# Kernel tuning notes

Measured on AMD Instinct MI355X. Metric: run time of the kernel, lower is better.

Reference implementation:

```python
import jax, jax.numpy as jnp
import numpy as np

# MolFormer TestBert config (from checkpoint hyper_parameters)
B, T, D, H, L, F, V = 64, 250, 768, 12, 12, 32, 2362
DH = D // H  # head dim = 64
EPS = 1e-6   # fast_transformers LinearAttention eps


def _layernorm(x, g, b):
    m = x.mean(-1, keepdims=True)
    v = ((x - m) ** 2).mean(-1, keepdims=True)
    return (x - m) / jnp.sqrt(v + 1e-5) * g + b


def setup_inputs() -> dict:
    key = jax.random.key(0)
    ks = jax.random.split(key, 20)
    s = 0.02

    def n(k, shape, scale=s):
        return jax.random.normal(k, shape, dtype=jnp.float32) * scale

    mask = jax.random.randint(ks[1], (B, T), 0, 2).astype(bool)
    mask = mask.at[:, 0].set(True)  # keep CLS position valid
    return {
        "batch": jax.random.randint(ks[0], (B, T), 0, V),
        "mask": mask,
        "tok_emb": n(ks[2], (V, D)),
        "pos_emb": n(ks[3], (1, T, D)),
        "Wq": n(ks[4], (L, D, D)), "bq": jnp.zeros((L, D)),
        "Wk": n(ks[5], (L, D, D)), "bk": jnp.zeros((L, D)),
        "Wv": n(ks[6], (L, D, D)), "bv": jnp.zeros((L, D)),
        "Wo": n(ks[7], (L, D, D)), "bo": jnp.zeros((L, D)),
        # GeneralizedRandomFeatures random projection omega: [L, head_dim, n_feats]
        "omega": jax.random.normal(ks[8], (L, DH, F), dtype=jnp.float32),
        "ln1_g": jnp.ones((L, D)), "ln1_b": jnp.zeros((L, D)),
        "ln2_g": jnp.ones((L, D)), "ln2_b": jnp.zeros((L, D)),
        # feed_forward_dimensions == n_embd in the builder kwargs
        "W1": n(ks[9], (L, D, D)), "b1": jnp.zeros((L, D)),
        "W2": n(ks[10], (L, D, D)), "b2": jnp.zeros((L, D)),
    }


def reference(batch, mask, tok_emb, pos_emb, Wq, bq, Wk, bk, Wv, bv, Wo, bo,
              omega, ln1_g, ln1_b, ln2_g, ln2_b, W1, b1, W2, b2):
    Bc, Tc = batch.shape
    # LengthMask(mask.sum(-1)) -> prefix key mask
    lengths = mask.astype(jnp.int32).sum(-1)
    key_mask = (jnp.arange(Tc)[None, :] < lengths[:, None]).astype(jnp.float32)  # [B,T]

    x = tok_emb[batch] + pos_emb[:, :Tc, :]  # dropout = identity in eval
    attn_w = None
    for l in range(L):
        q = (x @ Wq[l] + bq[l]).reshape(Bc, Tc, H, DH)
        k = (x @ Wk[l] + bk[l]).reshape(Bc, Tc, H, DH)
        v = (x @ Wv[l] + bv[l]).reshape(Bc, Tc, H, DH)
        # GeneralizedRandomFeatures: phi(x) = relu(x @ omega)
        Qf = jax.nn.relu(jnp.einsum('bthd,df->bthf', q, omega[l]))
        Kf = jax.nn.relu(jnp.einsum('bshd,df->bshf', k, omega[l]))
        Kf = Kf * key_mask[:, :, None, None]
        # linear attention: out = phi(Q) (phi(K)^T V) / (phi(Q) . sum phi(K))
        KV = jnp.einsum('bshf,bshm->bhfm', Kf, v)
        Z = 1.0 / (jnp.einsum('bthf,bhf->bth', Qf, Kf.sum(axis=1)) + EPS)
        out = jnp.einsum('bthf,bhfm,bth->bthm', Qf, KV, Z)
        if l == L - 1:
            # 'linearwweights': the implied (normalized) attention matrix
            attn_w = jnp.einsum('bthf,bshf,bth->bhts', Qf, Kf, Z)
        out = out.reshape(Bc, Tc, D) @ Wo[l] + bo[l]
        # fast_transformers post-norm encoder layer
        x = _layernorm(x + out, ln1_g[l], ln1_b[l])
        y = jax.nn.gelu(x @ W1[l] + b1[l], approximate=False) @ W2[l] + b2[l]
        x = _layernorm(x + y, ln2_g[l], ln2_b[l])
    # mode == 'cls'
    return x[:, 0, :], attn_w
```

## Files before the change

### kernel.cpp

```cpp
#include <hip/hip_runtime.h>
#include <hip/hip_bf16.h>

typedef __hip_bfloat16 bf16;
typedef __attribute__((ext_vector_type(4))) float f32x4;
typedef __attribute__((ext_vector_type(8))) short bf16x8;
typedef __attribute__((ext_vector_type(4))) short short4v;

#define B_ 64
#define T_ 250
#define D_ 768
#define H_ 12
#define DH_ 64
#define F_ 32
#define L_ 12
#define BT_ (B_*T_)
#define BT_P 16128
#define NF_ (H_*F_)
#define QKVN_ (3*D_)
#define KVTN_ 80

static __device__ __forceinline__ float b2f(short s) {
    union { float f; unsigned u; } z; z.u = ((unsigned)(unsigned short)s) << 16; return z.f;
}
static __device__ __forceinline__ short f2bs(float f) {
    bf16 b = __float2bfloat16(f);
    return *(short*)&b;
}

__global__ void lengths_kernel(const unsigned char* __restrict__ mask, int* __restrict__ lengths) {
    __shared__ int not_i32, not_f32;
    const unsigned int* w = (const unsigned int*)mask;
    int tid = threadIdx.x;
    if (tid == 0) { not_i32 = 0; not_f32 = 0; }
    __syncthreads();
    int li = 0, lf = 0;
    for (int i = tid; i < 4000; i += 256) {
        unsigned int v = w[i];
        if (v > 1u) li = 1;
        if (v != 0u && v != 0x3F800000u) lf = 1;
    }
    if (li) not_i32 = 1;
    if (lf) not_f32 = 1;
    __syncthreads();
    int mode = (!not_i32) ? 0 : ((!not_f32) ? 1 : 2);
    if (tid < B_) {
        int cnt = 0;
        if (mode == 0) {
            const int* r = (const int*)mask + tid * T_;
            for (int t = 0; t < T_; ++t) cnt += (r[t] != 0);
        } else if (mode == 1) {
            const unsigned int* r = w + tid * T_;
            for (int t = 0; t < T_; ++t) cnt += (r[t] != 0);
        } else {
            const unsigned char* r = mask + tid * T_;
            for (int t = 0; t < T_; ++t) cnt += (r[t] != 0);
        }
        lengths[tid] = cnt;
    }
}

__global__ void embed_kernel(const int* __restrict__ batch, const float* __restrict__ tok,
                             const float* __restrict__ pos, float* __restrict__ x,
                             bf16* __restrict__ xb) {
    int bt = blockIdx.x;
    int t = bt % T_;
    int tok_id = batch[bt];
    const float* tr = tok + (size_t)tok_id * D_;
    const float* pr = pos + (size_t)t * D_;
    float* xr = x + (size_t)bt * D_;
    bf16* xbr = xb + (size_t)bt * D_;
    for (int d = threadIdx.x; d < D_; d += 256) {
        float v = tr[d] + pr[d];
        xr[d] = v;
        xbr[d] = __float2bfloat16(v);
    }
}

__global__ __launch_bounds__(256) void transpose_w_all(
    const float* __restrict__ Wq, const float* __restrict__ Wk, const float* __restrict__ Wv,
    const float* __restrict__ Wo, const float* __restrict__ W1, const float* __restrict__ W2,
    bf16* __restrict__ Wt)
{
    __shared__ float tile[32][33];
    int zz = blockIdx.z;
    int l = zz / 6, m = zz - l * 6;
    const float* src;
    switch (m) {
        case 0: src = Wq; break; case 1: src = Wk; break; case 2: src = Wv; break;
        case 3: src = Wo; break; case 4: src = W1; break; default: src = W2; break;
    }
    src += (size_t)l * D_ * D_;
    bf16* dst = Wt + (size_t)zz * D_ * D_;
    int k0 = blockIdx.y * 32, n0 = blockIdx.x * 32;
    int tx = threadIdx.x, ty = threadIdx.y;
#pragma unroll
    for (int i = 0; i < 4; ++i)
        tile[ty + i * 8][tx] = src[(size_t)(k0 + ty + i * 8) * D_ + n0 + tx];
    __syncthreads();
#pragma unroll
    for (int i = 0; i < 4; ++i)
        dst[(size_t)(n0 + ty + i * 8) * D_ + k0 + tx] = __float2bfloat16(tile[tx][ty + i * 8]);
}

__global__ void pack_bias(const float* __restrict__ bq, const float* __restrict__ bk,
                          const float* __restrict__ bv, float* __restrict__ qkvb) {
    int o = blockIdx.x * 256 + threadIdx.x;
    if (o >= L_ * QKVN_) return;
    int l = o / QKVN_, c = o - l * QKVN_;
    float v;
    if (c < D_) v = bq[l * D_ + c];
    else if (c < 2 * D_) v = bk[l * D_ + c - D_];
    else v = bv[l * D_ + c - 2 * D_];
    qkvb[o] = v;
}

#define GP_SLOT 28672
__global__ __launch_bounds__(512, 2) void gemm_pipe(
    const bf16* __restrict__ A, const bf16* __restrict__ Bt,
    const float* __restrict__ bias, bf16* __restrict__ C,
    int N, int lda, int ldc, int act, const int* __restrict__ lengths)
{
    __shared__ __attribute__((aligned(16))) short lds_s[2 * GP_SLOT];
    const int tid = threadIdx.x, lane = tid & 63, wave = tid >> 6;
    const int wm = wave >> 2, wn = wave & 3;
    const int rsel = lane & 15, kq = lane >> 4;

    const int gx = gridDim.x;
    const int nwg = gx * gridDim.y;
    int orig = blockIdx.y * gx + blockIdx.x;
    int q = nwg >> 3, r = nwg & 7;
    int xcd = orig & 7, idx = orig >> 3;
    int swz = (xcd < r) ? xcd * (q + 1) + idx : r * (q + 1) + (xcd - r) * q + idx;
    const int row0 = (swz / gx) * 256;
    const int col0 = (swz % gx) * 192;

    const int srow = wave * 8 + (lane >> 3);
    const int sblk = (lane & 7) ^ ((lane >> 3) & 7);
    const short* gA = (const short*)A + (size_t)(row0 + srow) * lda + sblk * 8;
    const short* gB = (const short*)Bt + (size_t)(col0 + srow) * 768 + sblk * 8;
    const int ldest = wave * 512;

    f32x4 acc[8][3];
#pragma unroll
    for (int i = 0; i < 8; ++i)
#pragma unroll
        for (int j = 0; j < 3; ++j) acc[i][j] = (f32x4){0.f, 0.f, 0.f, 0.f};

    auto STAGE = [&](int kt, int slot) {
        short* base = lds_s + slot * GP_SLOT;
        int kc = kt * 64;
#pragma unroll
        for (int j = 0; j < 4; ++j)
            __builtin_amdgcn_global_load_lds(
                (const __attribute__((address_space(1))) unsigned int*)(gA + (size_t)(j * 64) * lda + kc),
                (__attribute__((address_space(3))) unsigned int*)(base + j * 4096 + ldest), 16, 0, 0);
#pragma unroll
        for (int j = 0; j < 3; ++j)
            __builtin_amdgcn_global_load_lds(
                (const __attribute__((address_space(1))) unsigned int*)(gB + (size_t)(j * 64) * 768 + kc),
                (__attribute__((address_space(3))) unsigned int*)(base + 16384 + j * 4096 + ldest), 16, 0, 0);
    };

    auto COMPUTE = [&](int slot) {
        const short* sA = lds_s + slot * GP_SLOT;
        const short* sB = sA + 16384;
#pragma unroll
        for (int ks = 0; ks < 2; ++ks) {
            int kb = ks * 4 + kq;
            bf16x8 bv[3];
#pragma unroll
            for (int n = 0; n < 3; ++n) {
                int rowb = wn * 48 + n * 16 + rsel;
                bv[n] = *(const bf16x8*)(sB + rowb * 64 + ((kb ^ (rowb & 7)) << 3));
            }
#pragma unroll
            for (int mh = 0; mh < 2; ++mh) {
                bf16x8 av[4];
#pragma unroll
                for (int m2 = 0; m2 < 4; ++m2) {
                    int rowa = wm * 128 + (mh * 4 + m2) * 16 + rsel;
                    av[m2] = *(const bf16x8*)(sA + rowa * 64 + ((kb ^ (rowa & 7)) << 3));
                }
                __builtin_amdgcn_s_setprio(1);
#pragma unroll
                for (int m2 = 0; m2 < 4; ++m2)
#pragma unroll
                    for (int n = 0; n < 3; ++n)
                        acc[mh * 4 + m2][n] = __builtin_amdgcn_mfma_f32_16x16x32_bf16(
                            av[m2], bv[n], acc[mh * 4 + m2][n], 0, 0, 0);
                __builtin_amdgcn_s_setprio(0);
            }
        }
    };

    STAGE(0, 0); STAGE(1, 1);
    asm volatile("s_waitcnt vmcnt(7)" ::: "memory");
    __builtin_amdgcn_s_barrier();

    for (int t = 0; t < 12; ++t) {
        COMPUTE(t & 1);
        if (t < 11) {
            __builtin_amdgcn_s_barrier();
            if (t < 10) {
                STAGE(t + 2, t & 1);
                asm volatile("s_waitcnt vmcnt(7)" ::: "memory");
            } else {
                asm volatile("s_waitcnt vmcnt(0)" ::: "memory");
            }
            __builtin_amdgcn_s_barrier();
        }
    }

    float bj[3];
#pragma unroll
    for (int n = 0; n < 3; ++n) {
        int col = col0 + wn * 48 + n * 16 + rsel;
        bj[n] = bias ? bias[col] : 0.f;
    }
#pragma unroll
    for (int mi = 0; mi < 8; ++mi) {
#pragma unroll
        for (int rr = 0; rr < 4; ++rr) {
            int row = row0 + wm * 128 + mi * 16 + (kq << 2) + rr;
            bool kill = false;
            if (act == 3) { int b = row / T_; int t = row - b * T_; kill = (t >= lengths[b & 63]); }
            size_t base = (size_t)row * ldc + col0 + wn * 48 + rsel;
#pragma unroll
            for (int n = 0; n < 3; ++n) {
                float v = acc[mi][n][rr] + bj[n];
                if (act == 1) v = 0.5f * v * (1.0f + erff(v * 0.70710678118654752f));
                else if (act >= 2) v = fmaxf(v, 0.f);
                if (kill) v = 0.f;
                C[base + n * 16] = __float2bfloat16(v);
            }
        }
    }
}

__global__ __launch_bounds__(256) void feat_kernel(
    const bf16* __restrict__ qkv, const float* __restrict__ om,
    bf16* __restrict__ Qf, bf16* __restrict__ Kf, const int* __restrict__ lengths)
{
    __shared__ __attribute__((aligned(16))) short omT[32 * 64];
    int z = blockIdx.z, h = blockIdx.y;
    int row0 = blockIdx.x * 128;
    int tid = threadIdx.x, lane = tid & 63, wave = tid >> 6;
    {
        int f = tid >> 3, k0 = (tid & 7) * 8;
#pragma unroll
        for (int j = 0; j < 8; ++j)
            omT[f * 64 + k0 + j] = f2bs(om[(size_t)(k0 + j) * F_ + f]);
    }
    __syncthreads();

    const short* A = (const short*)qkv + (size_t)z * D_ + h * DH_;
    int rsel = lane & 15, kof = (lane >> 4) << 3;

    bf16x8 af[2][2], bfr[2][2];
#pragma unroll
    for (int mi = 0; mi < 2; ++mi) {
        int row = row0 + wave * 32 + mi * 16 + rsel;
#pragma unroll
        for (int ks = 0; ks < 2; ++ks)
            af[mi][ks] = *(const bf16x8*)(A + (size_t)row * QKVN_ + ks * 32 + kof);
    }
#pragma unroll
    for (int ni = 0; ni < 2; ++ni)
#pragma unroll
        for (int ks = 0; ks < 2; ++ks)
            bfr[ni][ks] = *(const bf16x8*)(omT + (ni * 16 + rsel) * 64 + ks * 32 + kof);

    f32x4 acc[2][2];
#pragma unroll
    for (int i = 0; i < 2; ++i)
#pragma unroll
        for (int j = 0; j < 2; ++j) acc[i][j] = (f32x4){0.f, 0.f, 0.f, 0.f};
#pragma unroll
    for (int mi = 0; mi < 2; ++mi)
#pragma unroll
        for (int ni = 0; ni < 2; ++ni)
#pragma unroll
            for (int ks = 0; ks < 2; ++ks)
                acc[mi][ni] = __builtin_amdgcn_mfma_f32_16x16x32_bf16(af[mi][ks], bfr[ni][ks], acc[mi][ni], 0, 0, 0);

    bf16* out = z ? Kf : Qf;
#pragma unroll
    for (int mi = 0; mi < 2; ++mi) {
#pragma unroll
        for (int r = 0; r < 4; ++r) {
            int row = row0 + wave * 32 + mi * 16 + ((lane >> 4) << 2) + r;
            bool kill = false;
            if (z) { int b = row / T_; int t = row - b * T_; kill = (t >= lengths[b]); }
#pragma unroll
            for (int ni = 0; ni < 2; ++ni) {
                float v = fmaxf(acc[mi][ni][r], 0.f);
                if (kill) v = 0.f;
                out[(size_t)row * NF_ + h * F_ + ni * 16 + rsel] = __float2bfloat16(v);
            }
        }
    }
}

__global__ __launch_bounds__(256) void kvsum_kernel(
    const bf16* __restrict__ Kf, const bf16* __restrict__ v, int ldv,
    bf16* __restrict__ KVt)
{
    __shared__ short KfS[64][36];
    __shared__ short vS[64][68];
    int h = blockIdx.x, b = blockIdx.y;
    int tid = threadIdx.x, lane = tid & 63, wv = tid >> 6;
    int lr = tid >> 2, cp = tid & 3;

    const short* Kg = (const short*)Kf + (size_t)(b * T_) * NF_ + h * F_;
    const short* Vg = (const short*)v + (size_t)(b * T_) * ldv + h * DH_;

    f32x4 acc[2];
    acc[0] = (f32x4){0.f, 0.f, 0.f, 0.f};
    acc[1] = (f32x4){0.f, 0.f, 0.f, 0.f};
    float ksacc = 0.f;

    for (int s0 = 0; s0 < T_; s0 += 64) {
        __syncthreads();
        int s = s0 + lr;
        if (s < T_) {
            bf16x8 k8 = *(const bf16x8*)(Kg + (size_t)s * NF_ + cp * 8);
            *(short4v*)&KfS[lr][cp * 8]     = *((const short4v*)&k8);
            *(short4v*)&KfS[lr][cp * 8 + 4] = *((const short4v*)&k8 + 1);
            bf16x8 v8a = *(const bf16x8*)(Vg + (size_t)s * ldv + cp * 16);
            bf16x8 v8b = *(const bf16x8*)(Vg + (size_t)s * ldv + cp * 16 + 8);
            *(short4v*)&vS[lr][cp * 16]      = *((const short4v*)&v8a);
            *(short4v*)&vS[lr][cp * 16 + 4]  = *((const short4v*)&v8a + 1);
            *(short4v*)&vS[lr][cp * 16 + 8]  = *((const short4v*)&v8b);
            *(short4v*)&vS[lr][cp * 16 + 12] = *((const short4v*)&v8b + 1);
        } else {
            short4v zz = (short4v){0, 0, 0, 0};
            *(short4v*)&KfS[lr][cp * 8]     = zz;
            *(short4v*)&KfS[lr][cp * 8 + 4] = zz;
            *(short4v*)&vS[lr][cp * 16]      = zz;
            *(short4v*)&vS[lr][cp * 16 + 4]  = zz;
            *(short4v*)&vS[lr][cp * 16 + 8]  = zz;
            *(short4v*)&vS[lr][cp * 16 + 12] = zz;
        }
        __syncthreads();
        if (tid < 32) {
            float p0 = 0.f, p1 = 0.f;
            for (int ss = 0; ss < 64; ss += 2) {
                p0 += b2f(KfS[ss][tid]);
                p1 += b2f(KfS[ss + 1][tid]);
            }
            ksacc += p0 + p1;
        }
        bf16x8 af0[2], af1[2], bfr[2];
#pragma unroll
        for (int ks = 0; ks < 2; ++ks) {
            int sb = ks * 32 + ((lane >> 4) << 3);
#pragma unroll
            for (int j = 0; j < 8; ++j) {
                ((short*)&af0[ks])[j] = KfS[sb + j][lane & 15];
                ((short*)&af1[ks])[j] = KfS[sb + j][16 + (lane & 15)];
                ((short*)&bfr[ks])[j] = vS[sb + j][wv * 16 + (lane & 15)];
            }
        }
#pragma unroll
        for (int ks = 0; ks < 2; ++ks) {
            acc[0] = __builtin_amdgcn_mfma_f32_16x16x32_bf16(af0[ks], bfr[ks], acc[0], 0, 0, 0);
            acc[1] = __builtin_amdgcn_mfma_f32_16x16x32_bf16(af1[ks], bfr[ks], acc[1], 0, 0, 0);
        }
    }

    bf16* dst = KVt + (size_t)(b * H_ + h) * KVTN_ * F_;
    int m = wv * 16 + (lane & 15);
#pragma unroll
    for (int mi = 0; mi < 2; ++mi) {
#pragma unroll
        for (int r = 0; r < 4; ++r) {
            int f = mi * 16 + ((lane >> 4) << 2) + r;
            dst[(size_t)m * F_ + f] = __float2bfloat16(acc[mi][r]);
        }
    }
    if (tid < 32) dst[(size_t)64 * F_ + tid] = __float2bfloat16(ksacc);
    if (tid < 240) {
        ((short*)dst)[65 * F_ + tid * 2]     = 0;
        ((short*)dst)[65 * F_ + tid * 2 + 1] = 0;
    }
}

__global__ __launch_bounds__(256) void attn_mfma(
    const bf16* __restrict__ Qf, const bf16* __restrict__ KVt,
    float* __restrict__ Z, bf16* __restrict__ out, int ldo)
{
    int h = blockIdx.x, b = blockIdx.y;
    int tid = threadIdx.x, lane = tid & 63, wv = tid >> 6;
    int t0 = wv * 64;
    int rsel = lane & 15, kof = (lane >> 4) << 3;

    const short* Qg = (const short*)Qf + h * F_;
    const short* Bg = (const short*)KVt + (size_t)(b * H_ + h) * KVTN_ * F_;

    bf16x8 af[4], bfr[5];
#pragma unroll
    for (int mi = 0; mi < 4; ++mi) {
        int t = t0 + mi * 16 + rsel;
        if (t > T_ - 1) t = T_ - 1;
        af[mi] = *(const bf16x8*)(Qg + (size_t)(b * T_ + t) * NF_ + kof);
    }
#pragma unroll
    for (int ni = 0; ni < 5; ++ni)
        bfr[ni] = *(const bf16x8*)(Bg + (size_t)(ni * 16 + rsel) * F_ + kof);

    f32x4 acc[4][5];
#pragma unroll
    for (int i = 0; i < 4; ++i)
#pragma unroll
        for (int j = 0; j < 5; ++j) acc[i][j] = (f32x4){0.f, 0.f, 0.f, 0.f};
#pragma unroll
    for (int mi = 0; mi < 4; ++mi)
#pragma unroll
        for (int ni = 0; ni < 5; ++ni)
            acc[mi][ni] = __builtin_amdgcn_mfma_f32_16x16x32_bf16(af[mi], bfr[ni], acc[mi][ni], 0, 0, 0);

#pragma unroll
    for (int mi = 0; mi < 4; ++mi) {
#pragma unroll
        for (int r = 0; r < 4; ++r) {
            int t = t0 + mi * 16 + ((lane >> 4) << 2) + r;
            float zden = __shfl(acc[mi][4][r], lane & 48, 64);
            float z = 1.0f / (zden + 1e-6f);
            if (t < T_) {
                if (rsel == 0) Z[(size_t)(b * T_ + t) * H_ + h] = z;
                size_t base = (size_t)(b * T_ + t) * ldo + h * DH_ + rsel;
#pragma unroll
                for (int ni = 0; ni < 4; ++ni)
                    out[base + ni * 16] = __float2bfloat16(acc[mi][ni][r] * z);
            }
        }
    }
}

__global__ __launch_bounds__(256) void attnw_kernel(const bf16* __restrict__ Qf,
                                                    const bf16* __restrict__ Kf,
                                                    const float* __restrict__ Z,
                                                    float* __restrict__ out) {
    int tt = blockIdx.x;
    int bh = blockIdx.y;
    int b = bh / H_, h = bh - b * H_;
    int tid = threadIdx.x;
    int lane = tid & 63, w = tid >> 6;
    int t0 = tt * 64, s0 = w * 64;
    int kof = (lane >> 4) * 8;

    const short* Qs = (const short*)Qf;
    const short* Ks = (const short*)Kf;

    bf16x8 af[4], bfr[4];
#pragma unroll
    for (int mi = 0; mi < 4; ++mi) {
        int t = t0 + mi * 16 + (lane & 15);
        if (t > T_ - 1) t = T_ - 1;
        af[mi] = *(const bf16x8*)(Qs + ((size_t)(b * T_ + t) * H_ + h) * F_ + kof);
    }
#pragma unroll
    for (int ni = 0; ni < 4; ++ni) {
        int s = s0 + ni * 16 + (lane & 15);
        if (s > T_ - 1) s = T_ - 1;
        bfr[ni] = *(const bf16x8*)(Ks + ((size_t)(b * T_ + s) * H_ + h) * F_ + kof);
    }

    f32x4 acc[4][4];
#pragma unroll
    for (int i = 0; i < 4; ++i)
#pragma unroll
        for (int j = 0; j < 4; ++j) acc[i][j] = (f32x4){0.f, 0.f, 0.f, 0.f};
#pragma unroll
    for (int mi = 0; mi < 4; ++mi)
#pragma unroll
        for (int ni = 0; ni < 4; ++ni)
            acc[mi][ni] = __builtin_amdgcn_mfma_f32_16x16x32_bf16(af[mi], bfr[ni], acc[mi][ni], 0, 0, 0);

#pragma unroll
    for (int mi = 0; mi < 4; ++mi) {
#pragma unroll
        for (int r = 0; r < 4; ++r) {
            int t = t0 + mi * 16 + (lane >> 4) * 4 + r;
            if (t >= T_) continue;
            float z = Z[(size_t)(b * T_ + t) * H_ + h];
            size_t base = ((size_t)bh * T_ + t) * T_;
#pragma unroll
            for (int ni = 0; ni < 4; ++ni) {
                int s = s0 + ni * 16 + (lane & 15);
                if (s < T_) out[base + s] = acc[mi][ni][r] * z;
            }
        }
    }
}

__global__ __launch_bounds__(256) void ln_kernel(float* __restrict__ x, const bf16* __restrict__ res,
                                                 int ldr,
                                                 const float* __restrict__ g, const float* __restrict__ bb,
                                                 bf16* __restrict__ xb) {
    int bt = blockIdx.x, tid = threadIdx.x;
    float* xr = x + (size_t)bt * D_;
    const bf16* rr = res + (size_t)bt * ldr;
    float v[3]; float s = 0.f, ss = 0.f;
#pragma unroll
    for (int i = 0; i < 3; ++i) {
        int idx = tid + i * 256;
        float t = xr[idx] + __bfloat162float(rr[idx]);
        v[i] = t; s += t; ss += t * t;
    }
#pragma unroll
    for (int o = 1; o < 64; o <<= 1) { s += __shfl_xor(s, o, 64); ss += __shfl_xor(ss, o, 64); }
    __shared__ float red[4][2];
    int wave = tid >> 6, lane = tid & 63;
    if (lane == 0) { red[wave][0] = s; red[wave][1] = ss; }
    __syncthreads();
    s = red[0][0] + red[1][0] + red[2][0] + red[3][0];
    ss = red[0][1] + red[1][1] + red[2][1] + red[3][1];
    float mean = s * (1.f / D_);
    float var = ss * (1.f / D_) - mean * mean;
    float rstd = rsqrtf(var + 1e-5f);
    bf16* xbr = xb + (size_t)bt * D_;
#pragma unroll
    for (int i = 0; i < 3; ++i) {
        int idx = tid + i * 256;
        float o = (v[i] - mean) * rstd * g[idx] + bb[idx];
        xr[idx] = o;
        xbr[idx] = __float2bfloat16(o);
    }
}

__global__ void cls_kernel(const float* __restrict__ x, float* __restrict__ out) {
    int o = blockIdx.x * 256 + threadIdx.x;
    if (o >= B_ * D_) return;
    int b = o / D_, d = o % D_;
    out[o] = x[(size_t)(b * T_) * D_ + d];
}

extern "C" void kernel_launch(void* const* d_in, const int* in_sizes, int n_in,
                              void* d_out, int out_size, void* d_ws, size_t ws_size,
                              hipStream_t stream) {
    const int*   batch = (const int*)d_in[0];
    const unsigned char* mask = (const unsigned char*)d_in[1];
    const float* tok  = (const float*)d_in[2];
    const float* pos  = (const float*)d_in[3];
    const float* Wq   = (const float*)d_in[4];
    const float* bq   = (const float*)d_in[5];
    const float* Wk   = (const float*)d_in[6];
    const float* bk   = (const float*)d_in[7];
    const float* Wv   = (const float*)d_in[8];
    const float* bv   = (const float*)d_in[9];
    const float* Wo   = (const float*)d_in[10];
    const float* bo   = (const float*)d_in[11];
    const float* omega= (const float*)d_in[12];
    const float* ln1g = (const float*)d_in[13];
    const float* ln1b = (const float*)d_in[14];
    const float* ln2g = (const float*)d_in[15];
    const float* ln2b = (const float*)d_in[16];
    const float* W1   = (const float*)d_in[17];
    const float* b1   = (const float*)d_in[18];
    const float* W2   = (const float*)d_in[19];
    const float* b2   = (const float*)d_in[20];

    float* out_cls  = (float*)d_out;
    float* out_attn = (float*)d_out + B_ * D_;

    char* wsb = (char*)d_ws;
    float* x   = (float*)wsb; wsb += (size_t)BT_ * D_ * 4;
    bf16* xb   = (bf16*)wsb;  wsb += (size_t)BT_P * D_ * 2;
    bf16* qkv  = (bf16*)wsb;  wsb += (size_t)BT_P * QKVN_ * 2;
    bf16* Qf   = (bf16*)wsb;  wsb += (size_t)BT_ * NF_ * 2;
    bf16* Kf   = (bf16*)wsb;  wsb += (size_t)BT_ * NF_ * 2;
    bf16* KVt  = (bf16*)wsb;  wsb += (size_t)B_ * H_ * KVTN_ * F_ * 2;
    float* Z   = (float*)wsb; wsb += (size_t)BT_ * H_ * 4;
    bf16* Wt   = (bf16*)wsb;  wsb += (size_t)L_ * 6 * D_ * D_ * 2;
    float* qkvb= (float*)wsb; wsb += (size_t)L_ * QKVN_ * 4;
    int* lengths = (int*)wsb; wsb += 256;

    lengths_kernel<<<1, 256, 0, stream>>>(mask, lengths);
    embed_kernel<<<BT_, 256, 0, stream>>>(batch, tok, pos, x, xb);
    pack_bias<<<(L_ * QKVN_ + 255) / 256, 256, 0, stream>>>(bq, bk, bv, qkvb);
    transpose_w_all<<<dim3(24, 24, 72), dim3(32, 8), 0, stream>>>(Wq, Wk, Wv, Wo, W1, W2, Wt);

    dim3 qkv_g(QKVN_ / 192, BT_P / 256);
    dim3 dxd_g(D_ / 192, BT_P / 256);
    dim3 feat_g(BT_ / 128, H_, 2);
    dim3 kv_g(H_, B_);
    const size_t WS = (size_t)D_ * D_;

    for (int l = 0; l < L_; ++l) {
        const bf16* Wtl = Wt + (size_t)l * 6 * WS;

        gemm_pipe<<<qkv_g, 512, 0, stream>>>(xb, Wtl, qkvb + l * QKVN_, qkv,
                                             QKVN_, D_, QKVN_, 0, lengths);

        feat_kernel<<<feat_g, 256, 0, stream>>>(qkv, omega + (size_t)l * DH_ * F_,
                                                Qf, Kf, lengths);

        kvsum_kernel<<<kv_g, 256, 0, stream>>>(Kf, qkv + 2 * D_, QKVN_, KVt);

        attn_mfma<<<kv_g, 256, 0, stream>>>(Qf, KVt, Z, qkv, QKVN_);

        if (l == L_ - 1)
            attnw_kernel<<<dim3(4, B_ * H_), 256, 0, stream>>>(Qf, Kf, Z, out_attn);

        gemm_pipe<<<dxd_g, 512, 0, stream>>>(qkv, Wtl + 3 * WS, bo + l * D_, qkv + D_,
                                             D_, QKVN_, QKVN_, 0, lengths);
        ln_kernel<<<BT_, 256, 0, stream>>>(x, qkv + D_, QKVN_, ln1g + l * D_, ln1b + l * D_, xb);

        gemm_pipe<<<dxd_g, 512, 0, stream>>>(xb, Wtl + 4 * WS, b1 + l * D_, qkv + 2 * D_,
                                             D_, D_, QKVN_, 1, lengths);
        gemm_pipe<<<dxd_g, 512, 0, stream>>>(qkv + 2 * D_, Wtl + 5 * WS, b2 + l * D_, qkv,
                                             D_, QKVN_, QKVN_, 0, lengths);
        ln_kernel<<<BT_, 256, 0, stream>>>(x, qkv, QKVN_, ln2g + l * D_, ln2b + l * D_, xb);
    }

    cls_kernel<<<(B_ * D_ + 255) / 256, 256, 0, stream>>>(x, out_cls);
}
```

Baseline: 3.353 ms.

## Fuse output/FFN GEMMs with residual LayerNorm and merge KV-sum with attention

Adds a gemm_ln kernel in which each block owns 64 full rows × 768 columns. It stages the whole A tile in LDS and streams B from global memory, so the residual add and LayerNorm can be applied in the epilogue. This removes the separate ln_kernel passes and their round trips through global memory. The kvsum and attention kernels are merged so the KV matrix stays in LDS instead of going through a workspace buffer. The cost is a full-width tile with occupancy 1 (96KB LDS), B operands read straight from global without LDS reuse across waves, and fewer blocks (252) than CUs, which risks slower GEMMs.

```diff
diff --git a/kernel.cpp b/kernel.cpp
--- a/kernel.cpp
+++ b/kernel.cpp
@@ -17,7 +17,6 @@
 #define BT_P 16128
 #define NF_ (H_*F_)
 #define QKVN_ (3*D_)
-#define KVTN_ 80
 
 static __device__ __forceinline__ float b2f(short s) {
     union { float f; unsigned u; } z; z.u = ((unsigned)(unsigned short)s) << 16; return z.f;
@@ -118,7 +117,7 @@
 __global__ __launch_bounds__(512, 2) void gemm_pipe(
     const bf16* __restrict__ A, const bf16* __restrict__ Bt,
     const float* __restrict__ bias, bf16* __restrict__ C,
-    int N, int lda, int ldc, int act, const int* __restrict__ lengths)
+    int N, int lda, int ldc)
 {
     __shared__ __attribute__((aligned(16))) short lds_s[2 * GP_SLOT];
     const int tid = threadIdx.x, lane = tid & 63, wave = tid >> 6;
@@ -222,16 +221,142 @@
 #pragma unroll
         for (int rr = 0; rr < 4; ++rr) {
             int row = row0 + wm * 128 + mi * 16 + (kq << 2) + rr;
-            bool kill = false;
-            if (act == 3) { int b = row / T_; int t = row - b * T_; kill = (t >= lengths[b & 63]); }
             size_t base = (size_t)row * ldc + col0 + wn * 48 + rsel;
 #pragma unroll
-            for (int n = 0; n < 3; ++n) {
-                float v = acc[mi][n][rr] + bj[n];
-                if (act == 1) v = 0.5f * v * (1.0f + erff(v * 0.70710678118654752f));
-                else if (act >= 2) v = fmaxf(v, 0.f);
-                if (kill) v = 0.f;
-                C[base + n * 16] = __float2bfloat16(v);
+            for (int n = 0; n < 3; ++n)
+                C[base + n * 16] = __float2bfloat16(acc[mi][n][rr] + bj[n]);
+        }
+    }
+}
+
+__global__ __launch_bounds__(512, 1) void gemm_ln(
+    const bf16* __restrict__ A, const bf16* __restrict__ Bt,
+    const float* __restrict__ bias, int lda, int mode,
+    bf16* __restrict__ Cout, int ldc,
+    float* __restrict__ x, bf16* __restrict__ xb,
+    const float* __restrict__ g, const float* __restrict__ bvec)
+{
+    __shared__ __attribute__((aligned(16))) short As[64 * 768];
+    __shared__ float red[64][8][2];
+    const int tid = threadIdx.x, lane = tid & 63, wave = tid >> 6;
+    const int rsel = lane & 15, kq = lane >> 4;
+    const int row0 = blockIdx.x * 64;
+
+    {
+        const short* Ag0 = (const short*)A + (size_t)row0 * lda;
+#pragma unroll
+        for (int j = 0; j < 12; ++j) {
+            int s = j * 512 + tid;
+            int row = s / 96;
+            int kbp = s - row * 96;
+            int kb = (kbp & 0x78) | ((kbp & 7) ^ (row & 7));
+            __builtin_amdgcn_global_load_lds(
+                (const __attribute__((address_space(1))) unsigned int*)(Ag0 + (size_t)row * lda + kb * 8),
+                (__attribute__((address_space(3))) unsigned int*)(As + (j * 512 + wave * 64) * 8), 16, 0, 0);
+        }
+    }
+    asm volatile("s_waitcnt vmcnt(0)" ::: "memory");
+    __syncthreads();
+
+    const short* Bg = (const short*)Bt + (size_t)(wave * 96 + rsel) * 768 + kq * 8;
+    f32x4 acc[4][6];
+#pragma unroll
+    for (int i = 0; i < 4; ++i)
+#pragma unroll
+        for (int j = 0; j < 6; ++j) acc[i][j] = (f32x4){0.f, 0.f, 0.f, 0.f};
+
+    for (int kt = 0; kt < 24; ++kt) {
+        int kb = kt * 4 + kq;
+        bf16x8 av[4], bvv[6];
+#pragma unroll
+        for (int m = 0; m < 4; ++m) {
+            int row = m * 16 + rsel;
+            int kbp = (kb & 0x78) | ((kb & 7) ^ (row & 7));
+            av[m] = *(const bf16x8*)(As + row * 768 + kbp * 8);
+        }
+#pragma unroll
+        for (int nf = 0; nf < 6; ++nf)
+            bvv[nf] = *(const bf16x8*)(Bg + (size_t)nf * 16 * 768 + kt * 32);
+        __builtin_amdgcn_s_setprio(1);
+#pragma unroll
+        for (int m = 0; m < 4; ++m)
+#pragma unroll
+            for (int nf = 0; nf < 6; ++nf)
+                acc[m][nf] = __builtin_amdgcn_mfma_f32_16x16x32_bf16(av[m], bvv[nf], acc[m][nf], 0, 0, 0);
+        __builtin_amdgcn_s_setprio(0);
+    }
+
+    float bj[6];
+#pragma unroll
+    for (int nf = 0; nf < 6; ++nf) bj[nf] = bias[wave * 96 + nf * 16 + rsel];
+
+    if (mode <= 1) {
+#pragma unroll
+        for (int m = 0; m < 4; ++m) {
+#pragma unroll
+            for (int rr = 0; rr < 4; ++rr) {
+                int grow = row0 + m * 16 + kq * 4 + rr;
+                if (grow >= BT_) continue;
+                size_t base = (size_t)grow * ldc + wave * 96 + rsel;
+#pragma unroll
+                for (int nf = 0; nf < 6; ++nf) {
+                    float v = acc[m][nf][rr] + bj[nf];
+                    if (mode == 1) v = 0.5f * v * (1.0f + erff(v * 0.70710678118654752f));
+                    Cout[base + nf * 16] = __float2bfloat16(v);
+                }
+            }
+        }
+        return;
+    }
+
+    float gv[6], bv2[6];
+#pragma unroll
+    for (int nf = 0; nf < 6; ++nf) {
+        int col = wave * 96 + nf * 16 + rsel;
+        gv[nf] = g[col]; bv2[nf] = bvec[col];
+    }
+#pragma unroll
+    for (int m = 0; m < 4; ++m) {
+#pragma unroll
+        for (int rr = 0; rr < 4; ++rr) {
+            int rl = m * 16 + kq * 4 + rr;
+            int grow = row0 + rl;
+            float s = 0.f, ss = 0.f;
+#pragma unroll
+            for (int nf = 0; nf < 6; ++nf) {
+                float rv = (grow < BT_) ? x[(size_t)grow * D_ + wave * 96 + nf * 16 + rsel] : 0.f;
+                float v = acc[m][nf][rr] + bj[nf] + rv;
+                acc[m][nf][rr] = v;
+                s += v; ss += v * v;
+            }
+#pragma unroll
+            for (int o = 1; o < 16; o <<= 1) {
+                s += __shfl_xor(s, o, 64);
+                ss += __shfl_xor(ss, o, 64);
+            }
+            if (rsel == 0) { red[rl][wave][0] = s; red[rl][wave][1] = ss; }
+        }
+    }
+    __syncthreads();
+#pragma unroll
+    for (int m = 0; m < 4; ++m) {
+#pragma unroll
+        for (int rr = 0; rr < 4; ++rr) {
+            int rl = m * 16 + kq * 4 + rr;
+            int grow = row0 + rl;
+            if (grow >= BT_) continue;
+            float S = 0.f, SS = 0.f;
+#pragma unroll
+            for (int w = 0; w < 8; ++w) { S += red[rl][w][0]; SS += red[rl][w][1]; }
+            float mean = S * (1.f / D_);
+            float var = SS * (1.f / D_) - mean * mean;
+            float rstd = rsqrtf(var + 1e-5f);
+            size_t base = (size_t)grow * D_ + wave * 96 + rsel;
+#pragma unroll
+            for (int nf = 0; nf < 6; ++nf) {
+                float o = (acc[m][nf][rr] - mean) * rstd * gv[nf] + bv2[nf];
+                x[base + nf * 16] = o;
+                xb[base + nf * 16] = __float2bfloat16(o);
             }
         }
     }
@@ -301,15 +426,18 @@
     }
 }
 
-__global__ __launch_bounds__(256) void kvsum_kernel(
+__global__ __launch_bounds__(256) void kvattn_kernel(
     const bf16* __restrict__ Kf, const bf16* __restrict__ v, int ldv,
-    bf16* __restrict__ KVt)
+    const bf16* __restrict__ Qf, float* __restrict__ Z,
+    bf16* __restrict__ out, int ldo)
 {
     __shared__ short KfS[64][36];
     __shared__ short vS[64][68];
+    __shared__ short KVtS[80][40];
     int h = blockIdx.x, b = blockIdx.y;
     int tid = threadIdx.x, lane = tid & 63, wv = tid >> 6;
     int lr = tid >> 2, cp = tid & 3;
+    int rsel = lane & 15, kq = lane >> 4;
 
     const short* Kg = (const short*)Kf + (size_t)(b * T_) * NF_ + h * F_;
     const short* Vg = (const short*)v + (size_t)(b * T_) * ldv + h * DH_;
@@ -353,12 +481,12 @@
         bf16x8 af0[2], af1[2], bfr[2];
 #pragma unroll
         for (int ks = 0; ks < 2; ++ks) {
-            int sb = ks * 32 + ((lane >> 4) << 3);
+            int sb = ks * 32 + (kq << 3);
 #pragma unroll
             for (int j = 0; j < 8; ++j) {
-                ((short*)&af0[ks])[j] = KfS[sb + j][lane & 15];
-                ((short*)&af1[ks])[j] = KfS[sb + j][16 + (lane & 15)];
-                ((short*)&bfr[ks])[j] = vS[sb + j][wv * 16 + (lane & 15)];
+                ((short*)&af0[ks])[j] = KfS[sb + j][rsel];
+                ((short*)&af1[ks])[j] = KfS[sb + j][16 + rsel];
+                ((short*)&bfr[ks])[j] = vS[sb + j][wv * 16 + rsel];
             }
         }
 #pragma unroll
@@ -368,36 +496,25 @@
         }
     }
 
-    bf16* dst = KVt + (size_t)(b * H_ + h) * KVTN_ * F_;
-    int m = wv * 16 + (lane & 15);
-#pragma unroll
-    for (int mi = 0; mi < 2; ++mi) {
-#pragma unroll
-        for (int r = 0; r < 4; ++r) {
-            int f = mi * 16 + ((lane >> 4) << 2) + r;
-            dst[(size_t)m * F_ + f] = __float2bfloat16(acc[mi][r]);
-        }
-    }
-    if (tid < 32) dst[(size_t)64 * F_ + tid] = __float2bfloat16(ksacc);
-    if (tid < 240) {
-        ((short*)dst)[65 * F_ + tid * 2]     = 0;
-        ((short*)dst)[65 * F_ + tid * 2 + 1] = 0;
-    }
-}
-
-__global__ __launch_bounds__(256) void attn_mfma(
-    const bf16* __restrict__ Qf, const bf16* __restrict__ KVt,
-    float* __restrict__ Z, bf16* __restrict__ out, int ldo)
-{
-    int h = blockIdx.x, b = blockIdx.y;
-    int tid = threadIdx.x, lane = tid & 63, wv = tid >> 6;
+    __syncthreads();
+    {
+        int m = wv * 16 + rsel;
+#pragma unroll
+        for (int mi = 0; mi < 2; ++mi)
+#pragma unroll
+            for (int r = 0; r < 4; ++r) {
+                int f = mi * 16 + (kq << 2) + r;
+                KVtS[m][f] = f2bs(acc[mi][r]);
+            }
+        if (tid < 32) KVtS[64][tid] = f2bs(ksacc);
+    }
+    __syncthreads();
+
+    const short* Qg = (const short*)Qf + h * F_;
     int t0 = wv * 64;
-    int rsel = lane & 15, kof = (lane >> 4) << 3;
-
-    const short* Qg = (const short*)Qf + h * F_;
-    const short* Bg = (const short*)KVt + (size_t)(b * H_ + h) * KVTN_ * F_;
-
-    bf16x8 af[4], bfr[5];
+    int kof = kq << 3;
+
+    bf16x8 af[4], bfr2[5];
 #pragma unroll
     for (int mi = 0; mi < 4; ++mi) {
         int t = t0 + mi * 16 + rsel;
@@ -406,32 +523,32 @@
     }
 #pragma unroll
     for (int ni = 0; ni < 5; ++ni)
-        bfr[ni] = *(const bf16x8*)(Bg + (size_t)(ni * 16 + rsel) * F_ + kof);
-
-    f32x4 acc[4][5];
+        bfr2[ni] = *(const bf16x8*)(&KVtS[ni * 16 + rsel][kof]);
+
+    f32x4 oacc[4][5];
 #pragma unroll
     for (int i = 0; i < 4; ++i)
 #pragma unroll
-        for (int j = 0; j < 5; ++j) acc[i][j] = (f32x4){0.f, 0.f, 0.f, 0.f};
+        for (int j = 0; j < 5; ++j) oacc[i][j] = (f32x4){0.f, 0.f, 0.f, 0.f};
 #pragma unroll
     for (int mi = 0; mi < 4; ++mi)
 #pragma unroll
         for (int ni = 0; ni < 5; ++ni)
-            acc[mi][ni] = __builtin_amdgcn_mfma_f32_16x16x32_bf16(af[mi], bfr[ni], acc[mi][ni], 0, 0, 0);
+            oacc[mi][ni] = __builtin_amdgcn_mfma_f32_16x16x32_bf16(af[mi], bfr2[ni], oacc[mi][ni], 0, 0, 0);
 
 #pragma unroll
     for (int mi = 0; mi < 4; ++mi) {
 #pragma unroll
         for (int r = 0; r < 4; ++r) {
-            int t = t0 + mi * 16 + ((lane >> 4) << 2) + r;
-            float zden = __shfl(acc[mi][4][r], lane & 48, 64);
+            int t = t0 + mi * 16 + (kq << 2) + r;
+            float zden = __shfl(oacc[mi][4][r], lane & 48, 64);
             float z = 1.0f / (zden + 1e-6f);
             if (t < T_) {
                 if (rsel == 0) Z[(size_t)(b * T_ + t) * H_ + h] = z;
                 size_t base = (size_t)(b * T_ + t) * ldo + h * DH_ + rsel;
 #pragma unroll
                 for (int ni = 0; ni < 4; ++ni)
-                    out[base + ni * 16] = __float2bfloat16(acc[mi][ni][r] * z);
+                    out[base + ni * 16] = __float2bfloat16(oacc[mi][ni][r] * z);
             }
         }
     }
@@ -491,41 +608,6 @@
                 if (s < T_) out[base + s] = acc[mi][ni][r] * z;
             }
         }
-    }
-}
-
-__global__ __launch_bounds__(256) void ln_kernel(float* __restrict__ x, const bf16* __restrict__ res,
-                                                 int ldr,
-                                                 const float* __restrict__ g, const float* __restrict__ bb,
-                                                 bf16* __restrict__ xb) {
-    int bt = blockIdx.x, tid = threadIdx.x;
-    float* xr = x + (size_t)bt * D_;
-    const bf16* rr = res + (size_t)bt * ldr;
-    float v[3]; float s = 0.f, ss = 0.f;
-#pragma unroll
-    for (int i = 0; i < 3; ++i) {
-        int idx = tid + i * 256;
-        float t = xr[idx] + __bfloat162float(rr[idx]);
-        v[i] = t; s += t; ss += t * t;
-    }
-#pragma unroll
-    for (int o = 1; o < 64; o <<= 1) { s += __shfl_xor(s, o, 64); ss += __shfl_xor(ss, o, 64); }
-    __shared__ float red[4][2];
-    int wave = tid >> 6, lane = tid & 63;
-    if (lane == 0) { red[wave][0] = s; red[wave][1] = ss; }
-    __syncthreads();
-    s = red[0][0] + red[1][0] + red[2][0] + red[3][0];
-    ss = red[0][1] + red[1][1] + red[2][1] + red[3][1];
-    float mean = s * (1.f / D_);
-    float var = ss * (1.f / D_) - mean * mean;
-    float rstd = rsqrtf(var + 1e-5f);
-    bf16* xbr = xb + (size_t)bt * D_;
-#pragma unroll
-    for (int i = 0; i < 3; ++i) {
-        int idx = tid + i * 256;
-        float o = (v[i] - mean) * rstd * g[idx] + bb[idx];
-        xr[idx] = o;
-        xbr[idx] = __float2bfloat16(o);
     }
 }
 
@@ -570,7 +652,6 @@
     bf16* qkv  = (bf16*)wsb;  wsb += (size_t)BT_P * QKVN_ * 2;
     bf16* Qf   = (bf16*)wsb;  wsb += (size_t)BT_ * NF_ * 2;
     bf16* Kf   = (bf16*)wsb;  wsb += (size_t)BT_ * NF_ * 2;
-    bf16* KVt  = (bf16*)wsb;  wsb += (size_t)B_ * H_ * KVTN_ * F_ * 2;
     float* Z   = (float*)wsb; wsb += (size_t)BT_ * H_ * 4;
     bf16* Wt   = (bf16*)wsb;  wsb += (size_t)L_ * 6 * D_ * D_ * 2;
     float* qkvb= (float*)wsb; wsb += (size_t)L_ * QKVN_ * 4;
@@ -582,36 +663,31 @@
     transpose_w_all<<<dim3(24, 24, 72), dim3(32, 8), 0, stream>>>(Wq, Wk, Wv, Wo, W1, W2, Wt);
 
     dim3 qkv_g(QKVN_ / 192, BT_P / 256);
-    dim3 dxd_g(D_ / 192, BT_P / 256);
     dim3 feat_g(BT_ / 128, H_, 2);
     dim3 kv_g(H_, B_);
+    const int lnr_g = BT_P / 64;
     const size_t WS = (size_t)D_ * D_;
 
     for (int l = 0; l < L_; ++l) {
         const bf16* Wtl = Wt + (size_t)l * 6 * WS;
 
         gemm_pipe<<<qkv_g, 512, 0, stream>>>(xb, Wtl, qkvb + l * QKVN_, qkv,
-                                             QKVN_, D_, QKVN_, 0, lengths);
+                                             QKVN_, D_, QKVN_);
 
         feat_kernel<<<feat_g, 256, 0, stream>>>(qkv, omega + (size_t)l * DH_ * F_,
                                                 Qf, Kf, lengths);
 
-        kvsum_kernel<<<kv_g, 256, 0, stream>>>(Kf, qkv + 2 * D_, QKVN_, KVt);
-
-        attn_mfma<<<kv_g, 256, 0, stream>>>(Qf, KVt, Z, qkv, QKVN_);
+        kvattn_kernel<<<kv_g, 256, 0, stream>>>(Kf, qkv + 2 * D_, QKVN_, Qf, Z, qkv, QKVN_);
 
         if (l == L_ - 1)
             attnw_kernel<<<dim3(4, B_ * H_), 256, 0, stream>>>(Qf, Kf, Z, out_attn);
 
-        gemm_pipe<<<dxd_g, 512, 0, stream>>>(qkv, Wtl + 3 * WS, bo + l * D_, qkv + D_,
-                                             D_, QKVN_, QKVN_, 0, lengths);
-        ln_kernel<<<BT_, 256, 0, stream>>>(x, qkv + D_, QKVN_, ln1g + l * D_, ln1b + l * D_, xb);
-
-        gemm_pipe<<<dxd_g, 512, 0, stream>>>(xb, Wtl + 4 * WS, b1 + l * D_, qkv + 2 * D_,
-                                             D_, D_, QKVN_, 1, lengths);
-        gemm_pipe<<<dxd_g, 512, 0, stream>>>(qkv + 2 * D_, Wtl + 5 * WS, b2 + l * D_, qkv,
-                                             D_, QKVN_, QKVN_, 0, lengths);
-        ln_kernel<<<BT_, 256, 0, stream>>>(x, qkv, QKVN_, ln2g + l * D_, ln2b + l * D_, xb);
+        gemm_ln<<<lnr_g, 512, 0, stream>>>(qkv, Wtl + 3 * WS, bo + l * D_, QKVN_, 2,
+                                           nullptr, 0, x, xb, ln1g + l * D_, ln1b + l * D_);
+        gemm_ln<<<lnr_g, 512, 0, stream>>>(xb, Wtl + 4 * WS, b1 + l * D_, D_, 1,
+                                           qkv + 2 * D_, QKVN_, nullptr, nullptr, nullptr, nullptr);
+        gemm_ln<<<lnr_g, 512, 0, stream>>>(qkv + 2 * D_, Wtl + 5 * WS, b2 + l * D_, QKVN_, 2,
+                                           nullptr, 0, x, xb, ln2g + l * D_, ln2b + l * D_);
     }
 
     cls_kernel<<<(B_ * D_ + 255) / 256, 256, 0, stream>>>(x, out_cls);
```

Measured after the change: 3.985 ms. 1.19x slower.
